# Kernel tuning notes

Hardware: AMD Instinct MI355X
Metric: run time of the kernel (lower is better)

The kernel has to match this reference:

```python
import jax, jax.numpy as jnp
import numpy as np

IMG = 1280
NC = 80
REG_MAX = 16
CLS_GAIN, BOX_GAIN, DFL_GAIN = 0.5, 7.5, 1.5
TOPK, TAL_ALPHA, TAL_BETA = 10, 0.5, 6.0
EPS = 1e-9


def _make_anchors():
    pts, strs = [], []
    for s in (8, 16, 32):
        n = IMG // s
        c = (np.arange(n, dtype=np.float32) + 0.5) * s
        xx, yy = np.meshgrid(c, c)
        pts.append(np.stack([xx.ravel(), yy.ravel()], -1))
        strs.append(np.full((n * n, 1), s, np.float32))
    return np.concatenate(pts), np.concatenate(strs)


def setup_inputs() -> dict:
    key = jax.random.key(0)
    k = jax.random.split(key, 5)
    B, MGT = 16, 32
    anc_np, str_np = _make_anchors()
    N = anc_np.shape[0]  # 33600
    cls_logits = jax.random.normal(k[0], (B, N, NC), jnp.float32) - 2.0
    box_dist = jax.random.normal(k[1], (B, N, 4 * REG_MAX), jnp.float32)
    anchors = jnp.asarray(anc_np)
    strides = jnp.asarray(str_np)
    # decode boxes consistently with a DFL head (softmax-expectation * stride)
    proj = jnp.arange(REG_MAX, dtype=jnp.float32)
    d = jax.nn.softmax(box_dist.reshape(B, N, 4, REG_MAX), -1) @ proj  # (B,N,4) ltrb
    d = d * strides[None]
    box_decoded = jnp.concatenate([anchors[None] - d[..., :2], anchors[None] + d[..., 2:]], -1)
    # targets: [class, x1, y1, x2, y2]; last rows padded with class -1
    lab = jax.random.randint(k[2], (B, MGT), 0, NC).astype(jnp.float32)
    lab = jnp.where(jnp.arange(MGT)[None, :] < 24, lab, -1.0)
    cxy = jax.random.uniform(k[3], (B, MGT, 2), minval=64.0, maxval=IMG - 64.0)
    wh = jax.random.uniform(k[4], (B, MGT, 2), minval=16.0, maxval=320.0)
    xy1 = jnp.clip(cxy - wh / 2, 0.0, IMG)
    xy2 = jnp.clip(cxy + wh / 2, 0.0, IMG)
    targets = jnp.concatenate([lab[..., None], xy1, xy2], -1)
    return {"cls_logits": cls_logits, "box_dist": box_dist, "box_decoded": box_decoded,
            "targets": targets, "anchors": anchors, "strides": strides}


def _ciou(b1, b2, eps=1e-7):
    """CIoU between xyxy boxes; shapes broadcast; returns (...)."""
    x11, y11, x12, y12 = b1[..., 0], b1[..., 1], b1[..., 2], b1[..., 3]
    x21, y21, x22, y22 = b2[..., 0], b2[..., 1], b2[..., 2], b2[..., 3]
    w1, h1 = x12 - x11, y12 - y11
    w2, h2 = x22 - x21, y22 - y21
    iw = jnp.clip(jnp.minimum(x12, x22) - jnp.maximum(x11, x21), 0.0)
    ih = jnp.clip(jnp.minimum(y12, y22) - jnp.maximum(y11, y21), 0.0)
    inter = iw * ih
    union = w1 * h1 + w2 * h2 - inter + eps
    iou = inter / union
    cw = jnp.maximum(x12, x22) - jnp.minimum(x11, x21)  # enclosing box
    ch = jnp.maximum(y12, y22) - jnp.minimum(y11, y21)
    c2 = cw * cw + ch * ch + eps
    rho2 = ((x21 + x22 - x11 - x12) ** 2 + (y21 + y22 - y11 - y12) ** 2) / 4.0
    v = (4.0 / jnp.pi ** 2) * (jnp.arctan(w2 / (h2 + eps)) - jnp.arctan(w1 / (h1 + eps))) ** 2
    alpha = jax.lax.stop_gradient(v / (v - iou + (1.0 + eps)))
    return iou - (rho2 / c2 + v * alpha)


def _assign(scores, pboxes, anc, gt_labels, gt_bboxes, gt_mask):
    """TaskAlignedAssigner. scores (B,N,C) sigmoid, pboxes (B,N,4), anc (N,2),
    gt_labels (B,M) int, gt_bboxes (B,M,4), gt_mask (B,M) bool."""
    B, N, C = scores.shape
    M = gt_labels.shape[1]
    # candidates: anchor centers strictly inside GT boxes -> (B,M,N)
    lt = anc[None, None] - gt_bboxes[:, :, None, :2]
    rb = gt_bboxes[:, :, None, 2:] - anc[None, None]
    mask_in = jnp.minimum(lt.min(-1), rb.min(-1)) > EPS
    # alignment metric: score[gt_label]^alpha * CIoU^beta
    lab = jnp.clip(gt_labels, 0)
    s = jnp.take_along_axis(scores, jnp.broadcast_to(lab[:, None, :], (B, N, M)), axis=2)
    s = jnp.transpose(s, (0, 2, 1))  # (B,M,N)
    overlaps = jnp.clip(_ciou(gt_bboxes[:, :, None, :], pboxes[:, None, :, :]), 0.0)
    valid = mask_in & gt_mask[:, :, None]
    align = jnp.where(valid, (s ** TAL_ALPHA) * (overlaps ** TAL_BETA), 0.0)
    # top-k candidates per GT along anchors
    tv, ti = jax.lax.top_k(align, TOPK)  # (B,M,K)
    bi = jnp.arange(B)[:, None, None]
    mi = jnp.arange(M)[None, :, None]
    cnt = jnp.zeros((B, M, N), jnp.float32).at[bi, mi, ti].add(jnp.where(tv > EPS, 1.0, 0.0))
    mask_pos = (cnt > 0) & valid
    # resolve anchors matched to multiple GTs: keep highest-overlap GT
    multi = mask_pos.sum(1) > 1  # (B,N)
    best = jnp.argmax(overlaps, axis=1)  # (B,N)
    is_best = jnp.arange(M)[None, :, None] == best[:, None, :]
    mask_pos = jnp.where(multi[:, None, :], is_best, mask_pos)
    fg = mask_pos.any(1)  # (B,N)
    gt_idx = jnp.argmax(mask_pos.astype(jnp.float32), axis=1)  # (B,N)
    t_labels = jnp.take_along_axis(lab, gt_idx, axis=1)
    t_bboxes = jnp.take_along_axis(gt_bboxes, gt_idx[..., None], axis=1)  # (B,N,4)
    t_scores = jax.nn.one_hot(t_labels, C, dtype=jnp.float32) * fg[..., None].astype(jnp.float32)
    # normalize: per-GT max overlap / max alignment
    mp = mask_pos.astype(jnp.float32)
    am = align * mp
    pos_align = am.max(-1, keepdims=True)   # (B,M,1)
    pos_ov = (overlaps * mp).max(-1, keepdims=True)
    norm = (am * pos_ov / (pos_align + EPS)).max(1)  # (B,N)
    return t_labels, t_bboxes, t_scores * norm[..., None], fg


def _bce_logits(x, t):
    return jnp.clip(x, 0.0) - x * t + jnp.log1p(jnp.exp(-jnp.abs(x)))


def _forward(cls_logits, box_dist, box_decoded, targets, anchors, strides):
    B, N, _ = cls_logits.shape
    gt_labels = targets[..., 0].astype(jnp.int32)
    gt_bboxes = targets[..., 1:5]
    area = jnp.clip(gt_bboxes[..., 2] - gt_bboxes[..., 0], 0.0) * jnp.clip(gt_bboxes[..., 3] - gt_bboxes[..., 1], 0.0)
    gt_mask = (gt_labels >= 0) & (area > 0)
    sg = jax.lax.stop_gradient
    _, t_bboxes, t_scores, fg = _assign(jax.nn.sigmoid(sg(cls_logits)), sg(box_decoded),
                                        anchors, gt_labels, gt_bboxes, gt_mask)
    tss = jnp.maximum(t_scores.sum(), 1.0)
    # Varifocal loss (alpha=0.75, gamma=2.0), IoU-aware soft labels
    p = jax.nn.sigmoid(cls_logits)
    pos = (t_scores > 0).astype(jnp.float32)
    w = 0.75 * (p ** 2.0) * (1.0 - pos) + t_scores * pos
    loss_cls = (_bce_logits(cls_logits, t_scores) * w).sum() / tss
    # CIoU loss on foreground anchors, weighted by assigned score
    weight = t_scores.sum(-1) * fg.astype(jnp.float32)  # (B,N)
    iou = _ciou(box_decoded, t_bboxes)
    loss_iou = ((1.0 - iou) * weight).sum() / tss
    # DFL on ltrb distances in stride units
    t_ltrb = jnp.concatenate([anchors[None] - t_bboxes[..., :2],
                              t_bboxes[..., 2:] - anchors[None]], -1) / strides[None]
    t = jnp.clip(t_ltrb, 0.0, REG_MAX - 1 - 0.01)  # (B,N,4)
    tl = t.astype(jnp.int32)
    wl = (tl + 1).astype(jnp.float32) - t
    lp = jax.nn.log_softmax(box_dist.reshape(B, N, 4, REG_MAX), -1)
    ll = jnp.take_along_axis(lp, tl[..., None], -1)[..., 0]
    lr = jnp.take_along_axis(lp, (tl + 1)[..., None], -1)[..., 0]
    dfl = -(ll * wl + lr * (1.0 - wl)).mean(-1)  # (B,N)
    loss_dfl = (dfl * weight).sum() / tss
    total = (CLS_GAIN * loss_cls + BOX_GAIN * loss_iou + DFL_GAIN * loss_dfl) * B
    return total, CLS_GAIN * loss_cls, BOX_GAIN * loss_iou, DFL_GAIN * loss_dfl


def reference(cls_logits, box_dist, box_decoded, targets, anchors, strides):
    return _forward(cls_logits, box_dist, box_decoded, targets, anchors, strides)
```

## Files before the change

kernel.cpp:

```cpp
#include <hip/hip_runtime.h>
#include <math.h>

#define MGT 32
#define NCLS 80
#define TEPS 1e-9f
#define CEPS 1e-7f
#define CAPMAX 4096

__device__ __forceinline__ float ciou_pre(float ax1, float ay1, float ax2, float ay2,
                                          float awh, float aatan,
                                          float bx1, float by1, float bx2, float by2,
                                          float bwh, float batan) {
    float iw = fmaxf(fminf(ax2, bx2) - fmaxf(ax1, bx1), 0.f);
    float ih = fmaxf(fminf(ay2, by2) - fmaxf(ay1, by1), 0.f);
    float inter = iw * ih;
    float uni = awh + bwh - inter + CEPS;
    float iou = inter / uni;
    float cw = fmaxf(ax2, bx2) - fminf(ax1, bx1);
    float ch = fmaxf(ay2, by2) - fminf(ay1, by1);
    float c2 = cw * cw + ch * ch + CEPS;
    float dx = bx1 + bx2 - ax1 - ax2;
    float dy = by1 + by2 - ay1 - ay2;
    float rho2 = (dx * dx + dy * dy) * 0.25f;
    float dv = batan - aatan;
    float v = 0.405284734569351f * dv * dv;
    float alpha = v / (v - iou + (1.f + CEPS));
    return iou - (rho2 / c2 + v * alpha);
}

__device__ __forceinline__ float sigm_fast(float x) {
    return __builtin_amdgcn_rcpf(1.f + __expf(-x));
}

__global__ __launch_bounds__(256) void k_cand(const float* __restrict__ cls,
                                              const float* __restrict__ bdec,
                                              const float* __restrict__ tgt,
                                              const float* __restrict__ anc,
                                              unsigned long long* __restrict__ cand,
                                              unsigned* __restrict__ cnt,
                                              unsigned* __restrict__ selmask,
                                              unsigned* __restrict__ pos_al,
                                              unsigned* __restrict__ pos_ov,
                                              int Nv, int cap) {
    __shared__ float sx1[MGT], sy1[MGT], sx2[MGT], sy2[MGT];
    __shared__ float swh[MGT], satan[MGT];
    __shared__ int slab[MGT], svld[MGT];
    int b = blockIdx.y, tid = threadIdx.x;
    if (tid < MGT) {
        const float* t = tgt + ((size_t)b * MGT + tid) * 5;
        float lf = t[0];
        float x1 = t[1], y1 = t[2], x2 = t[3], y2 = t[4];
        sx1[tid] = x1; sy1[tid] = y1; sx2[tid] = x2; sy2[tid] = y2;
        float gw = x2 - x1, gh = y2 - y1;
        swh[tid] = gw * gh;
        satan[tid] = atanf(gw / (gh + CEPS));
        float area = fmaxf(gw, 0.f) * fmaxf(gh, 0.f);
        int lab = (int)lf;
        svld[tid] = (lab >= 0 && area > 0.f) ? 1 : 0;
        slab[tid] = lab < 0 ? 0 : lab;
        if (blockIdx.x == 0) {
            pos_al[b * MGT + tid] = 0u;
            pos_ov[b * MGT + tid] = 0u;
        }
    }
    __syncthreads();
    int n = blockIdx.x * 256 + tid;
    if (n >= Nv) return;
    size_t bn = (size_t)b * Nv + n;
    selmask[bn] = 0u;
    float4 p = reinterpret_cast<const float4*>(bdec)[bn];
    float2 a = reinterpret_cast<const float2*>(anc)[n];
    const float* crow = cls + bn * NCLS;
    float pw = p.z - p.x, ph = p.w - p.y;
    float pwh = pw * ph;
    float patan = 0.f; bool have_patan = false;
    int lane = tid & 63;
    for (int m = 0; m < MGT; ++m) {
        float al = 0.f;
        if (svld[m]) {
            float mn = fminf(fminf(a.x - sx1[m], a.y - sy1[m]),
                             fminf(sx2[m] - a.x, sy2[m] - a.y));
            if (mn > TEPS) {
                if (!have_patan) { patan = atanf(pw / (ph + CEPS)); have_patan = true; }
                float ov = fmaxf(ciou_pre(sx1[m], sy1[m], sx2[m], sy2[m],
                                          swh[m], satan[m],
                                          p.x, p.y, p.z, p.w, pwh, patan), 0.f);
                if (ov > 0.f) {
                    float s = sigm_fast(crow[slab[m]]);
                    float o2 = ov * ov;
                    al = __builtin_sqrtf(s) * o2 * o2 * o2;
                }
            }
        }
        unsigned long long msk = __ballot(al > 0.f);
        if (msk) {
            int leader = __ffsll((long long)msk) - 1;
            unsigned base = 0;
            if (lane == leader)
                base = atomicAdd(&cnt[b * MGT + m], (unsigned)__popcll(msk));
            base = __shfl(base, leader, 64);
            if (al > 0.f) {
                unsigned rank = (unsigned)__popcll(msk & ((1ull << lane) - 1ull));
                unsigned idx = base + rank;
                if ((int)idx < cap) {
                    unsigned long long key =
                        (((unsigned long long)__float_as_uint(al)) << 32) |
                        (unsigned)(0xFFFFFFFFu - (unsigned)n);
                    cand[((size_t)b * MGT + m) * cap + idx] = key;
                }
            }
        }
    }
}

__global__ __launch_bounds__(256) void k_topk2(const unsigned long long* __restrict__ cand,
                                               const unsigned* __restrict__ cnt,
                                               unsigned* __restrict__ selmask,
                                               int Nv, int cap) {
    __shared__ unsigned long long lv[2560];
    __shared__ unsigned long long warp_r[4];
    __shared__ unsigned long long winner_s;
    int bid = blockIdx.x;
    int b = bid / MGT, m = bid - b * MGT;
    int tid = threadIdx.x;
    int total = (int)cnt[bid];
    if (total > cap) total = cap;
    const unsigned long long* row = cand + (size_t)bid * cap;
    unsigned long long v[10];
#pragma unroll
    for (int i = 0; i < 10; ++i) v[i] = 0ull;
    for (int i = tid; i < total; i += 256) {
        unsigned long long key = row[i];
        if (key > v[0]) {
            unsigned long long cv = key; bool placed = false;
#pragma unroll
            for (int j = 0; j < 9; ++j) {
                if (!placed) {
                    if (cv > v[j + 1]) { v[j] = v[j + 1]; }
                    else { v[j] = cv; placed = true; }
                }
            }
            if (!placed) v[9] = cv;
        }
    }
#pragma unroll
    for (int i = 0; i < 10; ++i) lv[tid * 10 + i] = v[i];
    __syncthreads();
    int p = 9;
    for (int r = 0; r < 10; ++r) {
        unsigned long long cand_k = (p >= 0) ? lv[tid * 10 + p] : 0ull;
        unsigned long long w = cand_k;
#pragma unroll
        for (int s = 32; s > 0; s >>= 1) {
            unsigned long long o = __shfl_xor(w, s, 64);
            w = (o > w) ? o : w;
        }
        if ((tid & 63) == 0) warp_r[tid >> 6] = w;
        __syncthreads();
        if (tid == 0) {
            unsigned long long ww = warp_r[0];
            ww = (warp_r[1] > ww) ? warp_r[1] : ww;
            ww = (warp_r[2] > ww) ? warp_r[2] : ww;
            ww = (warp_r[3] > ww) ? warp_r[3] : ww;
            winner_s = ww;
            float wv = __uint_as_float((unsigned)(ww >> 32));
            if (wv > TEPS) {
                unsigned wi = 0xFFFFFFFFu - (unsigned)(ww & 0xFFFFFFFFull);
                atomicOr(&selmask[(size_t)b * Nv + wi], 1u << m);
            }
        }
        __syncthreads();
        unsigned long long win = winner_s;
        if (win == 0ull) break;
        if (p >= 0 && cand_k == win) --p;
        __syncthreads();
    }
}

__global__ __launch_bounds__(256) void k_resolve(const float* __restrict__ cls,
                                                 const float* __restrict__ bdec,
                                                 const float* __restrict__ tgt,
                                                 const float* __restrict__ anc,
                                                 const unsigned* __restrict__ selmask,
                                                 int* __restrict__ gtf,
                                                 float* __restrict__ amv,
                                                 float* __restrict__ crv,
                                                 unsigned* __restrict__ pos_al,
                                                 unsigned* __restrict__ pos_ov, int Nv) {
    __shared__ float sx1[MGT], sy1[MGT], sx2[MGT], sy2[MGT];
    __shared__ float swh[MGT], satan[MGT];
    __shared__ int slab[MGT], svld[MGT];
    int b = blockIdx.y, tid = threadIdx.x;
    if (tid < MGT) {
        const float* t = tgt + ((size_t)b * MGT + tid) * 5;
        float lf = t[0];
        float x1 = t[1], y1 = t[2], x2 = t[3], y2 = t[4];
        sx1[tid] = x1; sy1[tid] = y1; sx2[tid] = x2; sy2[tid] = y2;
        float gw = x2 - x1, gh = y2 - y1;
        swh[tid] = gw * gh;
        satan[tid] = atanf(gw / (gh + CEPS));
        float area = fmaxf(gw, 0.f) * fmaxf(gh, 0.f);
        int lab = (int)lf;
        svld[tid] = (lab >= 0 && area > 0.f) ? 1 : 0;
        slab[tid] = lab < 0 ? 0 : lab;
    }
    __syncthreads();
    int n = blockIdx.x * 256 + tid;
    if (n >= Nv) return;
    size_t bn = (size_t)b * Nv + n;
    unsigned msk = selmask[bn];
    if (!msk) { gtf[bn] = -1; amv[bn] = 0.f; crv[bn] = 0.f; return; }
    float4 p = reinterpret_cast<const float4*>(bdec)[bn];
    float pw = p.z - p.x, ph = p.w - p.y;
    float pwh = pw * ph;
    float patan = atanf(pw / (ph + CEPS));
    int g;
    if (__popc(msk) > 1) {
        float bo = -1.f; g = 0;
        for (int m = 0; m < MGT; ++m) {
            float ov = fmaxf(ciou_pre(sx1[m], sy1[m], sx2[m], sy2[m],
                                      swh[m], satan[m],
                                      p.x, p.y, p.z, p.w, pwh, patan), 0.f);
            if (ov > bo) { bo = ov; g = m; }
        }
    } else {
        g = __ffs(msk) - 1;
    }
    float cr = ciou_pre(sx1[g], sy1[g], sx2[g], sy2[g], swh[g], satan[g],
                        p.x, p.y, p.z, p.w, pwh, patan);
    float ov = fmaxf(cr, 0.f);
    float al = 0.f;
    if (svld[g]) {
        float2 a = reinterpret_cast<const float2*>(anc)[n];
        float mn = fminf(fminf(a.x - sx1[g], a.y - sy1[g]),
                         fminf(sx2[g] - a.x, sy2[g] - a.y));
        if (mn > TEPS && ov > 0.f) {
            float s = sigm_fast(cls[bn * NCLS + slab[g]]);
            float o2 = ov * ov;
            al = __builtin_sqrtf(s) * o2 * o2 * o2;
        }
    }
    gtf[bn] = g; amv[bn] = al; crv[bn] = cr;
    atomicMax(&pos_al[b * MGT + g], __float_as_uint(al));
    atomicMax(&pos_ov[b * MGT + g], __float_as_uint(ov));
}

__global__ __launch_bounds__(256) void k_boxdfl(const float* __restrict__ bdist,
                                                const float* __restrict__ tgt,
                                                const float* __restrict__ anc,
                                                const float* __restrict__ strd,
                                                const int* __restrict__ gtf,
                                                const float* __restrict__ amv,
                                                const float* __restrict__ crv,
                                                const unsigned* __restrict__ pos_al,
                                                const unsigned* __restrict__ pos_ov,
                                                float* __restrict__ tval,
                                                int* __restrict__ tlabv,
                                                float* __restrict__ p_tss,
                                                float* __restrict__ p_iou,
                                                float* __restrict__ p_dfl, int Nv) {
    __shared__ float sx1[MGT], sy1[MGT], sx2[MGT], sy2[MGT];
    __shared__ int slab[MGT];
    __shared__ float r0[256], r1[256], r2[256];
    int b = blockIdx.y, tid = threadIdx.x;
    if (tid < MGT) {
        const float* t = tgt + ((size_t)b * MGT + tid) * 5;
        float lf = t[0];
        sx1[tid] = t[1]; sy1[tid] = t[2]; sx2[tid] = t[3]; sy2[tid] = t[4];
        slab[tid] = lf < 0.f ? 0 : (int)lf;
    }
    __syncthreads();
    int n = blockIdx.x * 256 + tid;
    float c_t = 0.f, c_i = 0.f, c_d = 0.f;
    if (n < Nv) {
        size_t bn = (size_t)b * Nv + n;
        int g = gtf[bn];
        float nv = 0.f;
        if (g >= 0) {
            float pa = __uint_as_float(pos_al[b * MGT + g]);
            float po = __uint_as_float(pos_ov[b * MGT + g]);
            nv = amv[bn] * po / (pa + TEPS);
        }
        tval[bn] = nv;
        tlabv[bn] = (g >= 0) ? slab[g] : -1;
        if (nv > 0.f) {
            c_t = nv;
            c_i = (1.f - crv[bn]) * nv;
            float2 a = reinterpret_cast<const float2*>(anc)[n];
            float st = strd[n];
            float ttv[4];
            ttv[0] = (a.x - sx1[g]) / st;
            ttv[1] = (a.y - sy1[g]) / st;
            ttv[2] = (sx2[g] - a.x) / st;
            ttv[3] = (sy2[g] - a.y) / st;
            const float* bd = bdist + bn * 64;
            float acc = 0.f;
#pragma unroll
            for (int k = 0; k < 4; ++k) {
                float t = fminf(fmaxf(ttv[k], 0.f), 14.99f);
                int tl = (int)t;
                float wl = (float)(tl + 1) - t;
                float mx = -3.4e38f;
                for (int j = 0; j < 16; ++j) mx = fmaxf(mx, bd[k * 16 + j]);
                float se = 0.f;
                for (int j = 0; j < 16; ++j) se += __expf(bd[k * 16 + j] - mx);
                float lse = mx + __logf(se);
                float ll = bd[k * 16 + tl] - lse;
                float lr = bd[k * 16 + tl + 1] - lse;
                acc += ll * wl + lr * (1.f - wl);
            }
            c_d = (-acc * 0.25f) * nv;
        }
    }
    r0[tid] = c_t; r1[tid] = c_i; r2[tid] = c_d;
    __syncthreads();
    for (int s = 128; s > 0; s >>= 1) {
        if (tid < s) { r0[tid] += r0[tid + s]; r1[tid] += r1[tid + s]; r2[tid] += r2[tid + s]; }
        __syncthreads();
    }
    if (tid == 0) {
        int bi = blockIdx.y * gridDim.x + blockIdx.x;
        p_tss[bi] = r0[0]; p_iou[bi] = r1[0]; p_dfl[bi] = r2[0];
    }
}

__global__ __launch_bounds__(256) void k_cls2(const float* __restrict__ cls,
                                              const int* __restrict__ tlabv,
                                              const float* __restrict__ tval,
                                              float* __restrict__ p_cls,
                                              int total4, int stride_t) {
    __shared__ float rs[256];
    float sum = 0.f;
    for (int i4 = blockIdx.x * 256 + threadIdx.x; i4 < total4; i4 += stride_t) {
        int bn = i4 / 20;
        int pos = i4 - bn * 20;
        float4 x4 = reinterpret_cast<const float4*>(cls)[i4];
        int tlab = tlabv[bn];
        float tv = tval[bn];
        int c0 = pos * 4;
        float xs[4] = {x4.x, x4.y, x4.z, x4.w};
#pragma unroll
        for (int e = 0; e < 4; ++e) {
            float x = xs[e];
            float ea = __expf(-fabsf(x));
            float r = __builtin_amdgcn_rcpf(1.f + ea);
            float p = (x >= 0.f) ? r : ea * r;
            float t = (c0 + e == tlab) ? tv : 0.f;
            float bce = fmaxf(x, 0.f) - x * t + __logf(1.f + ea);
            float w = (t > 0.f) ? t : 0.75f * p * p;
            sum += bce * w;
        }
    }
    rs[threadIdx.x] = sum;
    __syncthreads();
    for (int s = 128; s > 0; s >>= 1) {
        if (threadIdx.x < s) rs[threadIdx.x] += rs[threadIdx.x + s];
        __syncthreads();
    }
    if (threadIdx.x == 0) p_cls[blockIdx.x] = rs[0];
}

__global__ __launch_bounds__(256) void k_final(const float* __restrict__ p_tss,
                                               const float* __restrict__ p_iou,
                                               const float* __restrict__ p_dfl,
                                               int nb,
                                               const float* __restrict__ p_cls,
                                               int ncb, float* __restrict__ out, int Bv) {
    __shared__ float s0[256], s1[256], s2[256], s3[256];
    int tid = threadIdx.x;
    float a0 = 0.f, a1 = 0.f, a2 = 0.f, a3 = 0.f;
    for (int i = tid; i < nb; i += 256) {
        a0 += p_tss[i]; a1 += p_iou[i]; a2 += p_dfl[i];
    }
    for (int i = tid; i < ncb; i += 256) a3 += p_cls[i];
    s0[tid] = a0; s1[tid] = a1; s2[tid] = a2; s3[tid] = a3;
    __syncthreads();
    for (int s = 128; s > 0; s >>= 1) {
        if (tid < s) { s0[tid] += s0[tid + s]; s1[tid] += s1[tid + s];
                       s2[tid] += s2[tid + s]; s3[tid] += s3[tid + s]; }
        __syncthreads();
    }
    if (tid == 0) {
        float tss = fmaxf(s0[0], 1.f);
        float lcls = 0.5f * s3[0] / tss;
        float liou = 7.5f * s1[0] / tss;
        float ldfl = 1.5f * s2[0] / tss;
        out[0] = (lcls + liou + ldfl) * (float)Bv;
        out[1] = lcls;
        out[2] = liou;
        out[3] = ldfl;
    }
}

extern "C" void kernel_launch(void* const* d_in, const int* in_sizes, int n_in,
                              void* d_out, int out_size, void* d_ws, size_t ws_size,
                              hipStream_t stream) {
    const float* cls = (const float*)d_in[0];
    const float* bdist = (const float*)d_in[1];
    const float* bdec = (const float*)d_in[2];
    const float* tgt = (const float*)d_in[3];
    const float* anc = (const float*)d_in[4];
    const float* strd = (const float*)d_in[5];
    int Nv = in_sizes[4] / 2;
    int Bv = in_sizes[3] / (MGT * 5);
    size_t nBN = (size_t)Bv * Nv;
    int gx = (Nv + 255) / 256;
    int nb = gx * Bv;
    int nbm = Bv * MGT;
    int total4 = (int)(nBN * (NCLS / 4));
    int ncb = 2048;
    if ((long long)ncb * 256 > (long long)total4) ncb = (total4 + 255) / 256;

    char* base = (char*)d_ws;
    size_t off = 0;
    unsigned* selmask = (unsigned*)(base + off); off += nBN * 4;
    unsigned* pos_al = (unsigned*)(base + off); off += (size_t)nbm * 4;
    unsigned* pos_ov = (unsigned*)(base + off); off += (size_t)nbm * 4;
    unsigned* cntv = (unsigned*)(base + off); off += (size_t)nbm * 4;
    int* gtfv = (int*)(base + off); off += nBN * 4;
    float* amv = (float*)(base + off); off += nBN * 4;
    float* crvv = (float*)(base + off); off += nBN * 4;
    float* tvalv = (float*)(base + off); off += nBN * 4;
    int* tlabv = (int*)(base + off); off += nBN * 4;
    float* p_tss = (float*)(base + off); off += (size_t)nb * 4;
    float* p_iou = (float*)(base + off); off += (size_t)nb * 4;
    float* p_dfl = (float*)(base + off); off += (size_t)nb * 4;
    float* p_cls = (float*)(base + off); off += (size_t)ncb * 4;
    off = (off + 7) & ~(size_t)7;
    unsigned long long* cand = (unsigned long long*)(base + off);
    size_t remain = (ws_size > off) ? (ws_size - off) : 0;
    int cap = (int)(remain / ((size_t)nbm * 8));
    if (cap > CAPMAX) cap = CAPMAX;
    if (cap < 1) cap = 1;

    dim3 grid(gx, Bv);
    hipMemsetAsync(cntv, 0, (size_t)nbm * 4, stream);
    k_cand<<<grid, 256, 0, stream>>>(cls, bdec, tgt, anc, cand, cntv,
                                     selmask, pos_al, pos_ov, Nv, cap);
    k_topk2<<<nbm, 256, 0, stream>>>(cand, cntv, selmask, Nv, cap);
    k_resolve<<<grid, 256, 0, stream>>>(cls, bdec, tgt, anc, selmask,
                                        gtfv, amv, crvv, pos_al, pos_ov, Nv);
    k_boxdfl<<<grid, 256, 0, stream>>>(bdist, tgt, anc, strd, gtfv, amv, crvv,
                                       pos_al, pos_ov, tvalv, tlabv,
                                       p_tss, p_iou, p_dfl, Nv);
    k_cls2<<<ncb, 256, 0, stream>>>(cls, tlabv, tvalv, p_cls, total4, ncb * 256);
    k_final<<<1, 256, 0, stream>>>(p_tss, p_iou, p_dfl, nb, p_cls, ncb,
                                   (float*)d_out, Bv);
}
```

Baseline: 121.0 us.

## Fuse box/DFL, class BCE and final reduction into one kernel

Merges k_boxdfl, k_cls2 and k_final into a single grid-stride kernel. It computes target scores inline per anchor, which removes the tval/tlab intermediate arrays, and finishes the reduction in the last block using an atomic done counter. The top-k kernel now keeps its per-thread candidate list in registers and shifts it, replacing the shared-memory staging. This saves two launches and the round-trip through intermediate global buffers. In exchange, gtf/amv are reloaded 20 times per anchor and the DFL work runs on only one lane out of each 20, which adds divergence.

```diff
diff --git a/kernel.cpp b/kernel.cpp
--- a/kernel.cpp
+++ b/kernel.cpp
@@ -117,7 +117,6 @@
                                                const unsigned* __restrict__ cnt,
                                                unsigned* __restrict__ selmask,
                                                int Nv, int cap) {
-    __shared__ unsigned long long lv[2560];
     __shared__ unsigned long long warp_r[4];
     __shared__ unsigned long long winner_s;
     int bid = blockIdx.x;
@@ -143,12 +142,8 @@
             if (!placed) v[9] = cv;
         }
     }
-#pragma unroll
-    for (int i = 0; i < 10; ++i) lv[tid * 10 + i] = v[i];
-    __syncthreads();
-    int p = 9;
     for (int r = 0; r < 10; ++r) {
-        unsigned long long cand_k = (p >= 0) ? lv[tid * 10 + p] : 0ull;
+        unsigned long long cand_k = v[9];
         unsigned long long w = cand_k;
 #pragma unroll
         for (int s = 32; s > 0; s >>= 1) {
@@ -172,7 +167,11 @@
         __syncthreads();
         unsigned long long win = winner_s;
         if (win == 0ull) break;
-        if (p >= 0 && cand_k == win) --p;
+        if (cand_k == win) {
+#pragma unroll
+            for (int j = 9; j > 0; --j) v[j] = v[j - 1];
+            v[0] = 0ull;
+        }
         __syncthreads();
     }
 }
@@ -245,55 +244,69 @@
     atomicMax(&pos_ov[b * MGT + g], __float_as_uint(ov));
 }
 
-__global__ __launch_bounds__(256) void k_boxdfl(const float* __restrict__ bdist,
-                                                const float* __restrict__ tgt,
-                                                const float* __restrict__ anc,
-                                                const float* __restrict__ strd,
-                                                const int* __restrict__ gtf,
-                                                const float* __restrict__ amv,
-                                                const float* __restrict__ crv,
-                                                const unsigned* __restrict__ pos_al,
-                                                const unsigned* __restrict__ pos_ov,
-                                                float* __restrict__ tval,
-                                                int* __restrict__ tlabv,
-                                                float* __restrict__ p_tss,
-                                                float* __restrict__ p_iou,
-                                                float* __restrict__ p_dfl, int Nv) {
-    __shared__ float sx1[MGT], sy1[MGT], sx2[MGT], sy2[MGT];
-    __shared__ int slab[MGT];
-    __shared__ float r0[256], r1[256], r2[256];
-    int b = blockIdx.y, tid = threadIdx.x;
-    if (tid < MGT) {
-        const float* t = tgt + ((size_t)b * MGT + tid) * 5;
-        float lf = t[0];
-        sx1[tid] = t[1]; sy1[tid] = t[2]; sx2[tid] = t[3]; sy2[tid] = t[4];
-        slab[tid] = lf < 0.f ? 0 : (int)lf;
-    }
-    __syncthreads();
-    int n = blockIdx.x * 256 + tid;
-    float c_t = 0.f, c_i = 0.f, c_d = 0.f;
-    if (n < Nv) {
-        size_t bn = (size_t)b * Nv + n;
+__global__ __launch_bounds__(256) void k_fused(const float* __restrict__ cls,
+                                               const float* __restrict__ bdist,
+                                               const float* __restrict__ tgt,
+                                               const float* __restrict__ anc,
+                                               const float* __restrict__ strd,
+                                               const int* __restrict__ gtf,
+                                               const float* __restrict__ amv,
+                                               const float* __restrict__ crv,
+                                               const unsigned* __restrict__ pos_al,
+                                               const unsigned* __restrict__ pos_ov,
+                                               float* __restrict__ p_cls,
+                                               float* __restrict__ p_tss,
+                                               float* __restrict__ p_iou,
+                                               float* __restrict__ p_dfl,
+                                               unsigned* __restrict__ done,
+                                               float* __restrict__ out,
+                                               int total4, int stride_t, int Nv, int Bv) {
+    __shared__ float r0[256], r1[256], r2[256], r3[256];
+    __shared__ int last_s;
+    int tid = threadIdx.x;
+    float s_cls = 0.f, s_tss = 0.f, s_iou = 0.f, s_dfl = 0.f;
+    for (int i4 = blockIdx.x * 256 + tid; i4 < total4; i4 += stride_t) {
+        int bn = i4 / 20;
+        int pos = i4 - bn * 20;
+        int b = bn / Nv;
         int g = gtf[bn];
         float nv = 0.f;
+        int tlab = -1;
         if (g >= 0) {
             float pa = __uint_as_float(pos_al[b * MGT + g]);
             float po = __uint_as_float(pos_ov[b * MGT + g]);
             nv = amv[bn] * po / (pa + TEPS);
-        }
-        tval[bn] = nv;
-        tlabv[bn] = (g >= 0) ? slab[g] : -1;
-        if (nv > 0.f) {
-            c_t = nv;
-            c_i = (1.f - crv[bn]) * nv;
+            float lf = tgt[((size_t)b * MGT + g) * 5];
+            tlab = lf < 0.f ? 0 : (int)lf;
+        }
+        float4 x4 = reinterpret_cast<const float4*>(cls)[i4];
+        int c0 = pos * 4;
+        float xs[4] = {x4.x, x4.y, x4.z, x4.w};
+#pragma unroll
+        for (int e = 0; e < 4; ++e) {
+            float x = xs[e];
+            float ea = __expf(-fabsf(x));
+            float r = __builtin_amdgcn_rcpf(1.f + ea);
+            float p = (x >= 0.f) ? r : ea * r;
+            float t = (c0 + e == tlab) ? nv : 0.f;
+            float bce = fmaxf(x, 0.f) - x * t + __logf(1.f + ea);
+            float w = (t > 0.f) ? t : 0.75f * p * p;
+            s_cls += bce * w;
+        }
+        if (pos == 0 && nv > 0.f) {
+            s_tss += nv;
+            s_iou += (1.f - crv[bn]) * nv;
+            int n = bn - b * Nv;
+            const float* t5 = tgt + ((size_t)b * MGT + g) * 5;
+            float x1 = t5[1], y1 = t5[2], x2 = t5[3], y2 = t5[4];
             float2 a = reinterpret_cast<const float2*>(anc)[n];
             float st = strd[n];
             float ttv[4];
-            ttv[0] = (a.x - sx1[g]) / st;
-            ttv[1] = (a.y - sy1[g]) / st;
-            ttv[2] = (sx2[g] - a.x) / st;
-            ttv[3] = (sy2[g] - a.y) / st;
-            const float* bd = bdist + bn * 64;
+            ttv[0] = (a.x - x1) / st;
+            ttv[1] = (a.y - y1) / st;
+            ttv[2] = (x2 - a.x) / st;
+            ttv[3] = (y2 - a.y) / st;
+            const float* bd = bdist + (size_t)bn * 64;
             float acc = 0.f;
 #pragma unroll
             for (int k = 0; k < 4; ++k) {
@@ -309,86 +322,53 @@
                 float lr = bd[k * 16 + tl + 1] - lse;
                 acc += ll * wl + lr * (1.f - wl);
             }
-            c_d = (-acc * 0.25f) * nv;
-        }
-    }
-    r0[tid] = c_t; r1[tid] = c_i; r2[tid] = c_d;
+            s_dfl += (-acc * 0.25f) * nv;
+        }
+    }
+    r0[tid] = s_cls; r1[tid] = s_tss; r2[tid] = s_iou; r3[tid] = s_dfl;
     __syncthreads();
     for (int s = 128; s > 0; s >>= 1) {
-        if (tid < s) { r0[tid] += r0[tid + s]; r1[tid] += r1[tid + s]; r2[tid] += r2[tid + s]; }
+        if (tid < s) { r0[tid] += r0[tid + s]; r1[tid] += r1[tid + s];
+                       r2[tid] += r2[tid + s]; r3[tid] += r3[tid + s]; }
         __syncthreads();
     }
     if (tid == 0) {
-        int bi = blockIdx.y * gridDim.x + blockIdx.x;
-        p_tss[bi] = r0[0]; p_iou[bi] = r1[0]; p_dfl[bi] = r2[0];
-    }
-}
-
-__global__ __launch_bounds__(256) void k_cls2(const float* __restrict__ cls,
-                                              const int* __restrict__ tlabv,
-                                              const float* __restrict__ tval,
-                                              float* __restrict__ p_cls,
-                                              int total4, int stride_t) {
-    __shared__ float rs[256];
-    float sum = 0.f;
-    for (int i4 = blockIdx.x * 256 + threadIdx.x; i4 < total4; i4 += stride_t) {
-        int bn = i4 / 20;
-        int pos = i4 - bn * 20;
-        float4 x4 = reinterpret_cast<const float4*>(cls)[i4];
-        int tlab = tlabv[bn];
-        float tv = tval[bn];
-        int c0 = pos * 4;
-        float xs[4] = {x4.x, x4.y, x4.z, x4.w};
-#pragma unroll
-        for (int e = 0; e < 4; ++e) {
-            float x = xs[e];
-            float ea = __expf(-fabsf(x));
-            float r = __builtin_amdgcn_rcpf(1.f + ea);
-            float p = (x >= 0.f) ? r : ea * r;
-            float t = (c0 + e == tlab) ? tv : 0.f;
-            float bce = fmaxf(x, 0.f) - x * t + __logf(1.f + ea);
-            float w = (t > 0.f) ? t : 0.75f * p * p;
-            sum += bce * w;
-        }
-    }
-    rs[threadIdx.x] = sum;
+        int bid = blockIdx.x;
+        p_cls[bid] = r0[0]; p_tss[bid] = r1[0];
+        p_iou[bid] = r2[0]; p_dfl[bid] = r3[0];
+        __threadfence();
+        unsigned prev = atomicAdd(done, 1u);
+        last_s = (prev == gridDim.x - 1) ? 1 : 0;
+    }
     __syncthreads();
-    for (int s = 128; s > 0; s >>= 1) {
-        if (threadIdx.x < s) rs[threadIdx.x] += rs[threadIdx.x + s];
+    if (last_s) {
+        __threadfence();
+        volatile const float* vc = p_cls;
+        volatile const float* vt = p_tss;
+        volatile const float* vi = p_iou;
+        volatile const float* vd = p_dfl;
+        int nbk = gridDim.x;
+        float a0 = 0.f, a1 = 0.f, a2 = 0.f, a3 = 0.f;
+        for (int i = tid; i < nbk; i += 256) {
+            a0 += vc[i]; a1 += vt[i]; a2 += vi[i]; a3 += vd[i];
+        }
+        r0[tid] = a0; r1[tid] = a1; r2[tid] = a2; r3[tid] = a3;
         __syncthreads();
-    }
-    if (threadIdx.x == 0) p_cls[blockIdx.x] = rs[0];
-}
-
-__global__ __launch_bounds__(256) void k_final(const float* __restrict__ p_tss,
-                                               const float* __restrict__ p_iou,
-                                               const float* __restrict__ p_dfl,
-                                               int nb,
-                                               const float* __restrict__ p_cls,
-                                               int ncb, float* __restrict__ out, int Bv) {
-    __shared__ float s0[256], s1[256], s2[256], s3[256];
-    int tid = threadIdx.x;
-    float a0 = 0.f, a1 = 0.f, a2 = 0.f, a3 = 0.f;
-    for (int i = tid; i < nb; i += 256) {
-        a0 += p_tss[i]; a1 += p_iou[i]; a2 += p_dfl[i];
-    }
-    for (int i = tid; i < ncb; i += 256) a3 += p_cls[i];
-    s0[tid] = a0; s1[tid] = a1; s2[tid] = a2; s3[tid] = a3;
-    __syncthreads();
-    for (int s = 128; s > 0; s >>= 1) {
-        if (tid < s) { s0[tid] += s0[tid + s]; s1[tid] += s1[tid + s];
-                       s2[tid] += s2[tid + s]; s3[tid] += s3[tid + s]; }
-        __syncthreads();
-    }
-    if (tid == 0) {
-        float tss = fmaxf(s0[0], 1.f);
-        float lcls = 0.5f * s3[0] / tss;
-        float liou = 7.5f * s1[0] / tss;
-        float ldfl = 1.5f * s2[0] / tss;
-        out[0] = (lcls + liou + ldfl) * (float)Bv;
-        out[1] = lcls;
-        out[2] = liou;
-        out[3] = ldfl;
+        for (int s = 128; s > 0; s >>= 1) {
+            if (tid < s) { r0[tid] += r0[tid + s]; r1[tid] += r1[tid + s];
+                           r2[tid] += r2[tid + s]; r3[tid] += r3[tid + s]; }
+            __syncthreads();
+        }
+        if (tid == 0) {
+            float tss = fmaxf(r1[0], 1.f);
+            float lcls = 0.5f * r0[0] / tss;
+            float liou = 7.5f * r2[0] / tss;
+            float ldfl = 1.5f * r3[0] / tss;
+            out[0] = (lcls + liou + ldfl) * (float)Bv;
+            out[1] = lcls;
+            out[2] = liou;
+            out[3] = ldfl;
+        }
     }
 }
 
@@ -405,7 +385,6 @@
     int Bv = in_sizes[3] / (MGT * 5);
     size_t nBN = (size_t)Bv * Nv;
     int gx = (Nv + 255) / 256;
-    int nb = gx * Bv;
     int nbm = Bv * MGT;
     int total4 = (int)(nBN * (NCLS / 4));
     int ncb = 2048;
@@ -417,14 +396,14 @@
     unsigned* pos_al = (unsigned*)(base + off); off += (size_t)nbm * 4;
     unsigned* pos_ov = (unsigned*)(base + off); off += (size_t)nbm * 4;
     unsigned* cntv = (unsigned*)(base + off); off += (size_t)nbm * 4;
+    unsigned* done = (unsigned*)(base + off); off += 8;
+    size_t zlen = (size_t)nbm * 4 + 8;
     int* gtfv = (int*)(base + off); off += nBN * 4;
     float* amv = (float*)(base + off); off += nBN * 4;
     float* crvv = (float*)(base + off); off += nBN * 4;
-    float* tvalv = (float*)(base + off); off += nBN * 4;
-    int* tlabv = (int*)(base + off); off += nBN * 4;
-    float* p_tss = (float*)(base + off); off += (size_t)nb * 4;
-    float* p_iou = (float*)(base + off); off += (size_t)nb * 4;
-    float* p_dfl = (float*)(base + off); off += (size_t)nb * 4;
+    float* p_tss = (float*)(base + off); off += (size_t)ncb * 4;
+    float* p_iou = (float*)(base + off); off += (size_t)ncb * 4;
+    float* p_dfl = (float*)(base + off); off += (size_t)ncb * 4;
     float* p_cls = (float*)(base + off); off += (size_t)ncb * 4;
     off = (off + 7) & ~(size_t)7;
     unsigned long long* cand = (unsigned long long*)(base + off);
@@ -434,16 +413,14 @@
     if (cap < 1) cap = 1;
 
     dim3 grid(gx, Bv);
-    hipMemsetAsync(cntv, 0, (size_t)nbm * 4, stream);
+    hipMemsetAsync(cntv, 0, zlen, stream);
     k_cand<<<grid, 256, 0, stream>>>(cls, bdec, tgt, anc, cand, cntv,
                                      selmask, pos_al, pos_ov, Nv, cap);
     k_topk2<<<nbm, 256, 0, stream>>>(cand, cntv, selmask, Nv, cap);
     k_resolve<<<grid, 256, 0, stream>>>(cls, bdec, tgt, anc, selmask,
                                         gtfv, amv, crvv, pos_al, pos_ov, Nv);
-    k_boxdfl<<<grid, 256, 0, stream>>>(bdist, tgt, anc, strd, gtfv, amv, crvv,
-                                       pos_al, pos_ov, tvalv, tlabv,
-                                       p_tss, p_iou, p_dfl, Nv);
-    k_cls2<<<ncb, 256, 0, stream>>>(cls, tlabv, tvalv, p_cls, total4, ncb * 256);
-    k_final<<<1, 256, 0, stream>>>(p_tss, p_iou, p_dfl, nb, p_cls, ncb,
-                                   (float*)d_out, Bv);
-}
+    k_fused<<<ncb, 256, 0, stream>>>(cls, bdist, tgt, anc, strd,
+                                     gtfv, amv, crvv, pos_al, pos_ov,
+                                     p_cls, p_tss, p_iou, p_dfl, done,
+                                     (float*)d_out, total4, ncb * 256, Nv, Bv);
+}
```

New measurement: 182.3 us. 50.6% more time.
